# Performance work log

Measured on AMD Instinct MI355X. Metric: run time of the kernel, lower is better.

The kernel has to match this reference:

```python
import jax, jax.numpy as jnp
import numpy as np

B, S, DIN, DOUT = 2, 4096, 4096, 16384

def setup_inputs() -> dict:
    key = jax.random.key(0)
    k1, k2, k3 = jax.random.split(key, 3)
    x = jax.random.normal(k1, (B, S, DIN), dtype=jnp.float32)
    weight = jax.random.normal(k2, (DOUT, DIN), dtype=jnp.float32) * 0.02
    bias = jax.random.normal(k3, (DOUT,), dtype=jnp.float32) * 0.01
    return {"x": x, "weight": weight, "bias": bias}

def reference(x, weight, bias):
    # per-tensor scale alpha = mean(|w|)
    alpha = jnp.mean(jnp.abs(weight))
    # ternary quantization: Q in {-1, 0, 1}
    Q = jnp.clip(jnp.round(weight / alpha), -1.0, 1.0)
    w_q = alpha * Q
    # STE: forward uses w_q, backward passes through to weight
    w_q = weight + jax.lax.stop_gradient(w_q - weight)
    # y = x @ w_q^T + b   (F.linear)
    return jnp.einsum('bsi,oi->bso', x, w_q) + bias
```

## Files before the change

### kernel.cpp

```cpp
#include <hip/hip_runtime.h>

#define M_DIM 8192
#define N_DIM 16384
#define K_DIM 4096
#define NT 64

typedef unsigned short u16;
typedef unsigned int u32;
typedef signed char s8;
typedef __attribute__((ext_vector_type(4))) int i32x4;
typedef __attribute__((ext_vector_type(8))) signed char s8x8;
typedef __attribute__((ext_vector_type(4))) float f32x4;

#define MFMAI8(a, b, c) __builtin_amdgcn_mfma_i32_16x16x64_i8(a, b, c, 0, 0, 0)
#define SGB(mask, n) __builtin_amdgcn_sched_group_barrier((mask), (n), 0)

__device__ __forceinline__ void gload16(const void* g, void* l) {
  __builtin_amdgcn_global_load_lds((const __attribute__((address_space(1))) void*)g,
                                   (__attribute__((address_space(3))) void*)l, 16, 0, 0);
}

__global__ void reduce_abs1(const float* __restrict__ w, double* __restrict__ partials) {
  const float4* w4 = (const float4*)w;
  size_t base = (size_t)blockIdx.x * 4096 + threadIdx.x;
  double s = 0.0;
#pragma unroll
  for (int i = 0; i < 16; ++i) {
    float4 v = w4[base + (size_t)i * 256];
    s += (double)fabsf(v.x); s += (double)fabsf(v.y);
    s += (double)fabsf(v.z); s += (double)fabsf(v.w);
  }
#pragma unroll
  for (int off = 32; off > 0; off >>= 1) s += __shfl_down(s, off, 64);
  __shared__ double red[4];
  int wv = threadIdx.x >> 6, lane = threadIdx.x & 63;
  if (lane == 0) red[wv] = s;
  __syncthreads();
  if (threadIdx.x == 0) partials[blockIdx.x] = (red[0] + red[1]) + (red[2] + red[3]);
}

__global__ void reduce_abs2(const double* __restrict__ partials,
                            double* __restrict__ alpha_d, float* __restrict__ alpha_f) {
  double s = 0.0;
  for (int i = threadIdx.x; i < 4096; i += 256) s += partials[i];
#pragma unroll
  for (int off = 32; off > 0; off >>= 1) s += __shfl_down(s, off, 64);
  __shared__ double red[4];
  int wv = threadIdx.x >> 6, lane = threadIdx.x & 63;
  if (lane == 0) red[wv] = s;
  __syncthreads();
  if (threadIdx.x == 0) {
    double total = (red[0] + red[1]) + (red[2] + red[3]);
    double a = total / (double)((long long)N_DIM * (long long)K_DIM);
    alpha_d[0] = a;
    alpha_f[0] = (float)a;
  }
}

__global__ void rowscale(const float* __restrict__ x, const float* __restrict__ alpha_f,
                         float* __restrict__ sinv, float* __restrict__ als) {
  const int row = blockIdx.x;
  const float4* x4 = (const float4*)(x + (size_t)row * K_DIM);
  float m = 0.f;
#pragma unroll
  for (int i = 0; i < 4; ++i) {
    float4 v = x4[threadIdx.x + i * 256];
    m = fmaxf(m, fmaxf(fmaxf(fabsf(v.x), fabsf(v.y)), fmaxf(fabsf(v.z), fabsf(v.w))));
  }
#pragma unroll
  for (int off = 32; off > 0; off >>= 1) m = fmaxf(m, __shfl_down(m, off, 64));
  __shared__ float red[4];
  int wv = threadIdx.x >> 6, lane = threadIdx.x & 63;
  if (lane == 0) red[wv] = m;
  __syncthreads();
  if (threadIdx.x == 0) {
    float mm = fmaxf(fmaxf(red[0], red[1]), fmaxf(red[2], red[3]));
    sinv[row] = 127.0f / mm;
    als[row] = alpha_f[0] * (mm / 127.0f);
  }
}

__global__ void prep_wx(const float* __restrict__ w, const float* __restrict__ x,
                        const double* __restrict__ alpha_d, const float* __restrict__ sinv,
                        s8* __restrict__ q, s8* __restrict__ xq) {
  const int b = blockIdx.x;
  if (b < 32768) {
    double inv = 1.0 / alpha_d[0];
    size_t i8i = (size_t)b * 256 + threadIdx.x;
    const float4* w4 = (const float4*)w;
    float4 v0 = w4[i8i * 2], v1 = w4[i8i * 2 + 1];
    float vv[8] = {v0.x, v0.y, v0.z, v0.w, v1.x, v1.y, v1.z, v1.w};
    s8x8 o;
#pragma unroll
    for (int j = 0; j < 8; ++j) {
      double r = rint((double)vv[j] * inv);
      s8 e = 0;
      if (r >= 1.0) e = 1;
      else if (r <= -1.0) e = -1;
      o[j] = e;
    }
    *((s8x8*)q + i8i) = o;
  } else {
    size_t i8i = (size_t)(b - 32768) * 256 + threadIdx.x;
    const int row = (b - 32768) >> 1;
    const float sv = sinv[row];
    const float4* x4 = (const float4*)x;
    float4 v0 = x4[i8i * 2], v1 = x4[i8i * 2 + 1];
    float vv[8] = {v0.x, v0.y, v0.z, v0.w, v1.x, v1.y, v1.z, v1.w};
    s8x8 o;
#pragma unroll
    for (int j = 0; j < 8; ++j) o[j] = (s8)(int)rintf(vv[j] * sv);
    *((s8x8*)xq + i8i) = o;
  }
}

__global__ __launch_bounds__(512, 2) void gemm_i8(
    const s8* __restrict__ A, const s8* __restrict__ Bq,
    const float* __restrict__ bias, const float* __restrict__ als,
    float* __restrict__ C) {
  __shared__ __align__(16) s8 Alds[4][256 * 64];
  __shared__ __align__(16) s8 Blds[4][256 * 64];

  const int t = threadIdx.x;
  const int wv = t >> 6, l = t & 63;
  const int wr = wv >> 2, wc = wv & 3;
  const int lr = l & 15, lk = l >> 4;

  const int bid = blockIdx.x;
  const int wg = (bid & 7) * 256 + (bid >> 3);
  const int grp = wg >> 9, rem = wg & 511;
  const int tm = grp * 8 + (rem & 7);
  const int tn = rem >> 3;

  const s8* Ag = A + (size_t)tm * 256 * K_DIM;
  const s8* Bg = Bq + (size_t)tn * 256 * K_DIM;

  int so[2], dof[2];
#pragma unroll
  for (int s = 0; s < 2; ++s) {
    int qch = s * 512 + t;
    int row = qch >> 2, c = (qch & 3) ^ ((row >> 1) & 3);
    so[s] = row * K_DIM + c * 16;
    dof[s] = (s * 512 + wv * 64) * 16;
  }

  const int fb = lr * 64 + ((lk ^ ((lr >> 1) & 3)) * 16);
#define LDA(b, m) (*(const i32x4*)(&Alds[b][wr * 8192 + (m) * 1024 + fb]))
#define LDB(b, n) (*(const i32x4*)(&Blds[b][wc * 4096 + (n) * 1024 + fb]))

  i32x4 acc[8][4];
#pragma unroll
  for (int mi = 0; mi < 8; ++mi)
#pragma unroll
    for (int ni = 0; ni < 4; ++ni)
      acc[mi][ni] = (i32x4){0, 0, 0, 0};

  auto stageA = [&](int g) {
    if (g < NT) {
      const s8* src = Ag + g * 64;
      gload16(src + so[0], &Alds[g & 3][dof[0]]);
      gload16(src + so[1], &Alds[g & 3][dof[1]]);
    }
  };
  auto stageB = [&](int g) {
    if (g < NT) {
      const s8* src = Bg + g * 64;
      gload16(src + so[0], &Blds[g & 3][dof[0]]);
      gload16(src + so[1], &Blds[g & 3][dof[1]]);
    }
  };

#define MFMA4(m0, m1, n0, n1)                                                  \
  acc[m0][n0] = MFMAI8(aF[m0], bF[n0], acc[m0][n0]);                           \
  acc[m0][n1] = MFMAI8(aF[m0], bF[n1], acc[m0][n1]);                           \
  acc[m1][n0] = MFMAI8(aF[m1], bF[n0], acc[m1][n0]);                           \
  acc[m1][n1] = MFMAI8(aF[m1], bF[n1], acc[m1][n1])

#define K_TILE(kt, b)                                                          \
  {                                                                            \
    i32x4 aF[8], bF[4];                                                        \
                                                         \
    aF[0] = LDA(b, 0); aF[1] = LDA(b, 1);                                      \
    bF[0] = LDB(b, 0); bF[1] = LDB(b, 1);                                      \
    SGB(0x100, 4);                                                             \
                               \
    aF[2] = LDA(b, 2); aF[3] = LDA(b, 3);                                      \
    bF[2] = LDB(b, 2);                                                         \
    stageA((kt) + 3);                                                          \
    MFMA4(0, 1, 0, 1);                                                         \
    SGB(0x100, 3); SGB(0x20, 2); SGB(0x8, 4);                                  \
                               \
    aF[4] = LDA(b, 4); aF[5] = LDA(b, 5);                                      \
    bF[3] = LDB(b, 3);                                                         \
    stageB((kt) + 3);                                                          \
    MFMA4(2, 3, 0, 1);                                                         \
    SGB(0x100, 3); SGB(0x20, 2); SGB(0x8, 4);                                  \
                                                 \
    aF[6] = LDA(b, 6); aF[7] = LDA(b, 7);                                      \
    MFMA4(0, 1, 2, 3);                                                         \
    SGB(0x100, 2); SGB(0x8, 4);                                                \
                                              \
    MFMA4(2, 3, 2, 3);                                                         \
    SGB(0x8, 4);                                                               \
    MFMA4(4, 5, 0, 1);                                                         \
    SGB(0x8, 4);                                                               \
    MFMA4(4, 5, 2, 3);                                                         \
    SGB(0x8, 4);                                                               \
    MFMA4(6, 7, 0, 1);                                                         \
    SGB(0x8, 4);                                                               \
    MFMA4(6, 7, 2, 3);                                                         \
    SGB(0x8, 4);                                                               \
            \
    if ((kt) < NT - 3) {                                                       \
      asm volatile("s_waitcnt vmcnt(8)" ::: "memory");                         \
      __builtin_amdgcn_s_barrier();                                            \
    } else if ((kt) == NT - 3) {                                               \
      asm volatile("s_waitcnt vmcnt(4)" ::: "memory");                         \
      __builtin_amdgcn_s_barrier();                                            \
    } else if ((kt) == NT - 2) {                                               \
      asm volatile("s_waitcnt vmcnt(0)" ::: "memory");                         \
      __builtin_amdgcn_s_barrier();                                            \
    }                                \
  }

  stageA(0); stageB(0);
  stageA(1); stageB(1);
  stageA(2); stageB(2);
  asm volatile("s_waitcnt vmcnt(8)" ::: "memory");
  __builtin_amdgcn_s_barrier();

  for (int kt4 = 0; kt4 < NT; kt4 += 4) {
    K_TILE(kt4 + 0, 0);
    K_TILE(kt4 + 1, 1);
    K_TILE(kt4 + 2, 2);
    K_TILE(kt4 + 3, 3);
  }
#undef K_TILE
#undef MFMA4
#undef LDA
#undef LDB

#pragma unroll
  for (int ni = 0; ni < 4; ++ni) {
    const int col = tn * 256 + wc * 64 + ni * 16 + lr;
    const float bs = bias[col];
#pragma unroll
    for (int mi = 0; mi < 8; ++mi) {
      const int rowbase = tm * 256 + wr * 128 + mi * 16 + lk * 4;
      const f32x4 av = *(const f32x4*)&als[rowbase];
      float* Cp = C + (size_t)rowbase * N_DIM + col;
#pragma unroll
      for (int j = 0; j < 4; ++j)
        Cp[(size_t)j * N_DIM] = av[j] * (float)acc[mi][ni][j] + bs;
    }
  }
}

extern "C" void kernel_launch(void* const* d_in, const int* in_sizes, int n_in,
                              void* d_out, int out_size, void* d_ws, size_t ws_size,
                              hipStream_t stream) {
  const float* x = (const float*)d_in[0];
  const float* w = (const float*)d_in[1];
  const float* bias = (const float*)d_in[2];
  float* out = (float*)d_out;

  char* ws = (char*)d_ws;
  double* alpha_d = (double*)ws;
  float* alpha_f = (float*)(ws + 8);
  double* partials = (double*)(ws + 16);
  float* sinv = (float*)(ws + 65536);
  float* als = (float*)(ws + 98304);
  s8* xq = (s8*)(ws + 131072);
  s8* qb = (s8*)(ws + 131072 + 33554432ULL);

  reduce_abs1<<<4096, 256, 0, stream>>>(w, partials);
  reduce_abs2<<<1, 256, 0, stream>>>(partials, alpha_d, alpha_f);
  rowscale<<<8192, 256, 0, stream>>>(x, alpha_f, sinv, als);
  prep_wx<<<49152, 256, 0, stream>>>(w, x, alpha_d, sinv, qb, xq);
  gemm_i8<<<2048, 512, 0, stream>>>(xq, qb, bias, als, out);
}
```

Measured before the change: 789.2 us.

## Use 1024-thread GEMM blocks with smaller per-wave tiles and fuse rowmax reduction

Doubles the GEMM workgroup to 16 waves, so each wave computes a 64x64 sub-tile with half the accumulators, and each thread issues one async LDS load per stage instead of two. Wait counts are adjusted to match. The row-max reduction of x is fused into the weight abs-sum kernel, removing one launch, and the per-row scales are folded into the quantize and epilogue steps. The trade is occupancy (one 1024-thread block per CU versus two 512-thread blocks) against lower register pressure and a different LDS-to-MFMA ratio per wave.

```diff
diff --git a/kernel.cpp b/kernel.cpp
--- a/kernel.cpp
+++ b/kernel.cpp
@@ -20,23 +20,43 @@
                                    (__attribute__((address_space(3))) void*)l, 16, 0, 0);
 }
 
-__global__ void reduce_abs1(const float* __restrict__ w, double* __restrict__ partials) {
-  const float4* w4 = (const float4*)w;
-  size_t base = (size_t)blockIdx.x * 4096 + threadIdx.x;
-  double s = 0.0;
-#pragma unroll
-  for (int i = 0; i < 16; ++i) {
-    float4 v = w4[base + (size_t)i * 256];
-    s += (double)fabsf(v.x); s += (double)fabsf(v.y);
-    s += (double)fabsf(v.z); s += (double)fabsf(v.w);
-  }
-#pragma unroll
-  for (int off = 32; off > 0; off >>= 1) s += __shfl_down(s, off, 64);
-  __shared__ double red[4];
-  int wv = threadIdx.x >> 6, lane = threadIdx.x & 63;
-  if (lane == 0) red[wv] = s;
-  __syncthreads();
-  if (threadIdx.x == 0) partials[blockIdx.x] = (red[0] + red[1]) + (red[2] + red[3]);
+__global__ void reduce_rowmax(const float* __restrict__ w, const float* __restrict__ x,
+                              double* __restrict__ partials, float* __restrict__ rowmax) {
+  if (blockIdx.x < 4096) {
+    const float4* w4 = (const float4*)w;
+    size_t base = (size_t)blockIdx.x * 4096 + threadIdx.x;
+    double s = 0.0;
+#pragma unroll
+    for (int i = 0; i < 16; ++i) {
+      float4 v = w4[base + (size_t)i * 256];
+      s += (double)fabsf(v.x); s += (double)fabsf(v.y);
+      s += (double)fabsf(v.z); s += (double)fabsf(v.w);
+    }
+#pragma unroll
+    for (int off = 32; off > 0; off >>= 1) s += __shfl_down(s, off, 64);
+    __shared__ double red[4];
+    int wv = threadIdx.x >> 6, lane = threadIdx.x & 63;
+    if (lane == 0) red[wv] = s;
+    __syncthreads();
+    if (threadIdx.x == 0) partials[blockIdx.x] = (red[0] + red[1]) + (red[2] + red[3]);
+  } else {
+    const int row = blockIdx.x - 4096;
+    const float4* x4 = (const float4*)(x + (size_t)row * K_DIM);
+    float m = 0.f;
+#pragma unroll
+    for (int i = 0; i < 4; ++i) {
+      float4 v = x4[threadIdx.x + i * 256];
+      m = fmaxf(m, fmaxf(fmaxf(fabsf(v.x), fabsf(v.y)), fmaxf(fabsf(v.z), fabsf(v.w))));
+    }
+#pragma unroll
+    for (int off = 32; off > 0; off >>= 1) m = fmaxf(m, __shfl_down(m, off, 64));
+    __shared__ float redf[4];
+    int wv = threadIdx.x >> 6, lane = threadIdx.x & 63;
+    if (lane == 0) redf[wv] = m;
+    __syncthreads();
+    if (threadIdx.x == 0)
+      rowmax[row] = fmaxf(fmaxf(redf[0], redf[1]), fmaxf(redf[2], redf[3]));
+  }
 }
 
 __global__ void reduce_abs2(const double* __restrict__ partials,
@@ -57,31 +77,8 @@
   }
 }
 
-__global__ void rowscale(const float* __restrict__ x, const float* __restrict__ alpha_f,
-                         float* __restrict__ sinv, float* __restrict__ als) {
-  const int row = blockIdx.x;
-  const float4* x4 = (const float4*)(x + (size_t)row * K_DIM);
-  float m = 0.f;
-#pragma unroll
-  for (int i = 0; i < 4; ++i) {
-    float4 v = x4[threadIdx.x + i * 256];
-    m = fmaxf(m, fmaxf(fmaxf(fabsf(v.x), fabsf(v.y)), fmaxf(fabsf(v.z), fabsf(v.w))));
-  }
-#pragma unroll
-  for (int off = 32; off > 0; off >>= 1) m = fmaxf(m, __shfl_down(m, off, 64));
-  __shared__ float red[4];
-  int wv = threadIdx.x >> 6, lane = threadIdx.x & 63;
-  if (lane == 0) red[wv] = m;
-  __syncthreads();
-  if (threadIdx.x == 0) {
-    float mm = fmaxf(fmaxf(red[0], red[1]), fmaxf(red[2], red[3]));
-    sinv[row] = 127.0f / mm;
-    als[row] = alpha_f[0] * (mm / 127.0f);
-  }
-}
-
 __global__ void prep_wx(const float* __restrict__ w, const float* __restrict__ x,
-                        const double* __restrict__ alpha_d, const float* __restrict__ sinv,
+                        const double* __restrict__ alpha_d, const float* __restrict__ rowmax,
                         s8* __restrict__ q, s8* __restrict__ xq) {
   const int b = blockIdx.x;
   if (b < 32768) {
@@ -103,7 +100,7 @@
   } else {
     size_t i8i = (size_t)(b - 32768) * 256 + threadIdx.x;
     const int row = (b - 32768) >> 1;
-    const float sv = sinv[row];
+    const float sv = 127.0f / rowmax[row];
     const float4* x4 = (const float4*)x;
     float4 v0 = x4[i8i * 2], v1 = x4[i8i * 2 + 1];
     float vv[8] = {v0.x, v0.y, v0.z, v0.w, v1.x, v1.y, v1.z, v1.w};
@@ -114,16 +111,16 @@
   }
 }
 
-__global__ __launch_bounds__(512, 2) void gemm_i8(
+__global__ __launch_bounds__(1024) void gemm_i8(
     const s8* __restrict__ A, const s8* __restrict__ Bq,
-    const float* __restrict__ bias, const float* __restrict__ als,
-    float* __restrict__ C) {
+    const float* __restrict__ bias, const float* __restrict__ alpha_f,
+    const float* __restrict__ rowmax, float* __restrict__ C) {
   __shared__ __align__(16) s8 Alds[4][256 * 64];
   __shared__ __align__(16) s8 Blds[4][256 * 64];
 
   const int t = threadIdx.x;
   const int wv = t >> 6, l = t & 63;
-  const int wr = wv >> 2, wc = wv & 3;
+  const int wr = wv >> 2, wcn = wv & 3;
   const int lr = l & 15, lk = l >> 4;
 
   const int bid = blockIdx.x;
@@ -135,39 +132,26 @@
   const s8* Ag = A + (size_t)tm * 256 * K_DIM;
   const s8* Bg = Bq + (size_t)tn * 256 * K_DIM;
 
-  int so[2], dof[2];
-#pragma unroll
-  for (int s = 0; s < 2; ++s) {
-    int qch = s * 512 + t;
-    int row = qch >> 2, c = (qch & 3) ^ ((row >> 1) & 3);
-    so[s] = row * K_DIM + c * 16;
-    dof[s] = (s * 512 + wv * 64) * 16;
-  }
+  const int srow = t >> 2, sc = (t & 3) ^ ((srow >> 1) & 3);
+  const int so = srow * K_DIM + sc * 16;
+  const int dof = wv * 1024;
 
   const int fb = lr * 64 + ((lk ^ ((lr >> 1) & 3)) * 16);
-#define LDA(b, m) (*(const i32x4*)(&Alds[b][wr * 8192 + (m) * 1024 + fb]))
-#define LDB(b, n) (*(const i32x4*)(&Blds[b][wc * 4096 + (n) * 1024 + fb]))
-
-  i32x4 acc[8][4];
-#pragma unroll
-  for (int mi = 0; mi < 8; ++mi)
+#define LDA(b, m) (*(const i32x4*)(&Alds[b][(wr * 4 + (m)) * 1024 + fb]))
+#define LDB(b, n) (*(const i32x4*)(&Blds[b][(wcn * 4 + (n)) * 1024 + fb]))
+
+  i32x4 acc[4][4];
+#pragma unroll
+  for (int mi = 0; mi < 4; ++mi)
 #pragma unroll
     for (int ni = 0; ni < 4; ++ni)
       acc[mi][ni] = (i32x4){0, 0, 0, 0};
 
   auto stageA = [&](int g) {
-    if (g < NT) {
-      const s8* src = Ag + g * 64;
-      gload16(src + so[0], &Alds[g & 3][dof[0]]);
-      gload16(src + so[1], &Alds[g & 3][dof[1]]);
-    }
+    if (g < NT) gload16(Ag + (size_t)g * 64 + so, &Alds[g & 3][dof]);
   };
   auto stageB = [&](int g) {
-    if (g < NT) {
-      const s8* src = Bg + g * 64;
-      gload16(src + so[0], &Blds[g & 3][dof[0]]);
-      gload16(src + so[1], &Blds[g & 3][dof[1]]);
-    }
+    if (g < NT) gload16(Bg + (size_t)g * 64 + so, &Blds[g & 3][dof]);
   };
 
 #define MFMA4(m0, m1, n0, n1)                                                  \
@@ -178,7 +162,7 @@
 
 #define K_TILE(kt, b)                                                          \
   {                                                                            \
-    i32x4 aF[8], bF[4];                                                        \
+    i32x4 aF[4], bF[4];                                                        \
                                                          \
     aF[0] = LDA(b, 0); aF[1] = LDA(b, 1);                                      \
     bF[0] = LDB(b, 0); bF[1] = LDB(b, 1);                                      \
@@ -188,34 +172,24 @@
     bF[2] = LDB(b, 2);                                                         \
     stageA((kt) + 3);                                                          \
     MFMA4(0, 1, 0, 1);                                                         \
-    SGB(0x100, 3); SGB(0x20, 2); SGB(0x8, 4);                                  \
-                               \
-    aF[4] = LDA(b, 4); aF[5] = LDA(b, 5);                                      \
+    SGB(0x100, 3); SGB(0x20, 1); SGB(0x8, 4);                                  \
+                                     \
     bF[3] = LDB(b, 3);                                                         \
     stageB((kt) + 3);                                                          \
     MFMA4(2, 3, 0, 1);                                                         \
-    SGB(0x100, 3); SGB(0x20, 2); SGB(0x8, 4);                                  \
-                                                 \
-    aF[6] = LDA(b, 6); aF[7] = LDA(b, 7);                                      \
+    SGB(0x100, 1); SGB(0x20, 1); SGB(0x8, 4);                                  \
+                                                           \
     MFMA4(0, 1, 2, 3);                                                         \
-    SGB(0x100, 2); SGB(0x8, 4);                                                \
-                                              \
+    SGB(0x8, 4);                                                               \
+                                                           \
     MFMA4(2, 3, 2, 3);                                                         \
     SGB(0x8, 4);                                                               \
-    MFMA4(4, 5, 0, 1);                                                         \
-    SGB(0x8, 4);                                                               \
-    MFMA4(4, 5, 2, 3);                                                         \
-    SGB(0x8, 4);                                                               \
-    MFMA4(6, 7, 0, 1);                                                         \
-    SGB(0x8, 4);                                                               \
-    MFMA4(6, 7, 2, 3);                                                         \
-    SGB(0x8, 4);                                                               \
-            \
+          \
     if ((kt) < NT - 3) {                                                       \
-      asm volatile("s_waitcnt vmcnt(8)" ::: "memory");                         \
+      asm volatile("s_waitcnt vmcnt(4)" ::: "memory");                         \
       __builtin_amdgcn_s_barrier();                                            \
     } else if ((kt) == NT - 3) {                                               \
-      asm volatile("s_waitcnt vmcnt(4)" ::: "memory");                         \
+      asm volatile("s_waitcnt vmcnt(2)" ::: "memory");                         \
       __builtin_amdgcn_s_barrier();                                            \
     } else if ((kt) == NT - 2) {                                               \
       asm volatile("s_waitcnt vmcnt(0)" ::: "memory");                         \
@@ -226,7 +200,7 @@
   stageA(0); stageB(0);
   stageA(1); stageB(1);
   stageA(2); stageB(2);
-  asm volatile("s_waitcnt vmcnt(8)" ::: "memory");
+  asm volatile("s_waitcnt vmcnt(4)" ::: "memory");
   __builtin_amdgcn_s_barrier();
 
   for (int kt4 = 0; kt4 < NT; kt4 += 4) {
@@ -240,18 +214,19 @@
 #undef LDA
 #undef LDB
 
+  const float aw = alpha_f[0] * (1.0f / 127.0f);
 #pragma unroll
   for (int ni = 0; ni < 4; ++ni) {
-    const int col = tn * 256 + wc * 64 + ni * 16 + lr;
+    const int col = tn * 256 + wcn * 64 + ni * 16 + lr;
     const float bs = bias[col];
 #pragma unroll
-    for (int mi = 0; mi < 8; ++mi) {
-      const int rowbase = tm * 256 + wr * 128 + mi * 16 + lk * 4;
-      const f32x4 av = *(const f32x4*)&als[rowbase];
+    for (int mi = 0; mi < 4; ++mi) {
+      const int rowbase = tm * 256 + wr * 64 + mi * 16 + lk * 4;
+      const f32x4 rm = *(const f32x4*)&rowmax[rowbase];
       float* Cp = C + (size_t)rowbase * N_DIM + col;
 #pragma unroll
       for (int j = 0; j < 4; ++j)
-        Cp[(size_t)j * N_DIM] = av[j] * (float)acc[mi][ni][j] + bs;
+        Cp[(size_t)j * N_DIM] = aw * rm[j] * (float)acc[mi][ni][j] + bs;
     }
   }
 }
@@ -268,14 +243,12 @@
   double* alpha_d = (double*)ws;
   float* alpha_f = (float*)(ws + 8);
   double* partials = (double*)(ws + 16);
-  float* sinv = (float*)(ws + 65536);
-  float* als = (float*)(ws + 98304);
+  float* rowmax = (float*)(ws + 65536);
   s8* xq = (s8*)(ws + 131072);
   s8* qb = (s8*)(ws + 131072 + 33554432ULL);
 
-  reduce_abs1<<<4096, 256, 0, stream>>>(w, partials);
+  reduce_rowmax<<<12288, 256, 0, stream>>>(w, x, partials, rowmax);
   reduce_abs2<<<1, 256, 0, stream>>>(partials, alpha_d, alpha_f);
-  rowscale<<<8192, 256, 0, stream>>>(x, alpha_f, sinv, als);
-  prep_wx<<<49152, 256, 0, stream>>>(w, x, alpha_d, sinv, qb, xq);
-  gemm_i8<<<2048, 512, 0, stream>>>(xq, qb, bias, als, out);
-}
+  prep_wx<<<49152, 256, 0, stream>>>(w, x, alpha_d, rowmax, qb, xq);
+  gemm_i8<<<2048, 1024, 0, stream>>>(xq, qb, bias, alpha_f, rowmax, out);
+}
```

Result: slower. 812.5 us (+3.0%).
